# Kernel optimization log

Hardware: AMD Instinct MI355X
Metric: run time of the kernel (lower is better)

The kernel has to match this reference:

```python
import jax, jax.numpy as jnp
import numpy as np

B, S, D, H = 2, 2048, 1024, 16
HD = D // H  # 64
NEG = 1.0e9


def setup_inputs() -> dict:
    key = jax.random.key(0)
    ks = jax.random.split(key, 9)
    scale = 1.0 / np.sqrt(D)
    return {
        "q_in": jax.random.normal(ks[0], (B, S, D), jnp.float32),
        "k_in": jax.random.normal(ks[1], (B, S, D), jnp.float32),
        "v_in": jax.random.normal(ks[2], (B, S, D), jnp.float32),
        "Wq": jax.random.normal(ks[3], (D, D), jnp.float32) * scale,
        "bq": jnp.zeros((D,), jnp.float32),
        "Wk": jax.random.normal(ks[4], (D, D), jnp.float32) * scale,
        "bk": jnp.zeros((D,), jnp.float32),
        "Wv": jax.random.normal(ks[5], (D, D), jnp.float32) * scale,
        "bv": jnp.zeros((D,), jnp.float32),
        "Wo": jax.random.normal(ks[6], (D, D), jnp.float32) * scale,
        "bo": jnp.zeros((D,), jnp.float32),
    }


def _split_heads(x):
    # [B,S,D] -> [B,H,S,HD]
    return x.reshape(B, S, H, HD).transpose(0, 2, 1, 3)


def reference(q_in, k_in, v_in, Wq, bq, Wk, bk, Wv, bv, Wo, bo):
    q = _split_heads(q_in @ Wq + bq)
    k = _split_heads(k_in @ Wk + bk)
    v = _split_heads(v_in @ Wv + bv)
    # scaled dot-product attention with additive causal mask (use_causal_mask=True)
    scores = jnp.einsum("bhqd,bhkd->bhqk", q, k) / jnp.sqrt(jnp.float32(HD))
    causal = jnp.tril(jnp.ones((S, S), jnp.float32))  # band_part(ones, -1, 0)
    scores = scores + (causal - 1.0) * NEG
    weights = jax.nn.softmax(scores, axis=-1)
    attn = jnp.einsum("bhqk,bhkd->bhqd", weights, v)
    concat = attn.transpose(0, 2, 1, 3).reshape(B, S, D)
    return concat @ Wo + bo
```

## Files before the change

kernel.cpp:

```cpp
#include <hip/hip_runtime.h>

#define B_  2
#define S_  2048
#define D_  1024
#define H_  16
#define HD_ 64
#define MM  (B_ * S_)

typedef __bf16 bf16;
typedef __attribute__((ext_vector_type(8))) __bf16 bf16x8;
typedef __attribute__((ext_vector_type(4))) __bf16 bf16x4;
typedef __attribute__((ext_vector_type(4))) float  f32x4;

__device__ inline float exp2g(float x) { return __builtin_amdgcn_exp2f(x); }

__device__ inline bf16x8 load8(const bf16* p) { return *(const bf16x8*)p; }
__device__ inline bf16x8 load8(const float* p) {
  float4 a = *(const float4*)p;
  float4 b = *(const float4*)(p + 4);
  bf16x8 r;
  r[0] = (bf16)a.x; r[1] = (bf16)a.y; r[2] = (bf16)a.z; r[3] = (bf16)a.w;
  r[4] = (bf16)b.x; r[5] = (bf16)b.y; r[6] = (bf16)b.z; r[7] = (bf16)b.w;
  return r;
}

__device__ inline void gld16(void* lds, const void* g) {
  __builtin_amdgcn_global_load_lds(
      (const __attribute__((address_space(1))) unsigned int*)g,
      (__attribute__((address_space(3))) unsigned int*)lds, 16, 0, 0);
}

__global__ __launch_bounds__(256) void transpose_w(
    const float* __restrict__ W0, const float* __restrict__ W1,
    const float* __restrict__ W2, const float* __restrict__ W3,
    bf16* __restrict__ T0, bf16* __restrict__ T1,
    bf16* __restrict__ T2, bf16* __restrict__ T3,
    const float* __restrict__ X0, const float* __restrict__ X1,
    const float* __restrict__ X2,
    bf16* __restrict__ Y0, bf16* __restrict__ Y1, bf16* __restrict__ Y2) {
  const int z = blockIdx.z;
  if (z >= 4) {
    const int p = z - 4, t = p >> 2;
    const float* src = t == 0 ? X0 : t == 1 ? X1 : X2;
    bf16* dst = t == 0 ? Y0 : t == 1 ? Y1 : Y2;
    long base = ((long)(p & 3) << 20) +
                (long)(blockIdx.y * 32 + blockIdx.x) * 1024 + threadIdx.x * 4;
    float4 v = *(const float4*)&src[base];
    bf16x4 o4;
    o4[0] = (bf16)v.x; o4[1] = (bf16)v.y; o4[2] = (bf16)v.z; o4[3] = (bf16)v.w;
    *(bf16x4*)&dst[base] = o4;
    return;
  }
  __shared__ bf16 t[32][40];
  const float* in = z == 0 ? W0 : z == 1 ? W1 : z == 2 ? W2 : W3;
  bf16* out = z == 0 ? T0 : z == 1 ? T1 : z == 2 ? T2 : T3;
  const int tx = threadIdx.x & 31;
  const int ty = threadIdx.x >> 5;
  const int r0 = blockIdx.y * 32, c0 = blockIdx.x * 32;
#pragma unroll
  for (int j = 0; j < 32; j += 8)
    t[ty + j][tx] = (bf16)in[(long)(r0 + ty + j) * D_ + (c0 + tx)];
  __syncthreads();
#pragma unroll
  for (int j = 0; j < 32; j += 8)
    out[(long)(c0 + ty + j) * D_ + (r0 + tx)] = t[tx][ty + j];
}

__global__ __launch_bounds__(256) void transpose_v64(const bf16* __restrict__ V,
                                                     bf16* __restrict__ VT) {
  __shared__ bf16 t[64][72];
  const int tid = threadIdx.x;
  const int s0 = blockIdx.x * 64;
  const int bh = blockIdx.y;
  const int b = bh >> 4, h = bh & 15;
  const bf16* ip = V + (long)b * S_ * D_ + h * HD_;
  bf16* op = VT + (long)bh * HD_ * S_;
#pragma unroll
  for (int i = 0; i < 2; ++i) {
    int c = tid + i * 256;
    int r = c >> 3, cc = (c & 7) * 8;
    *(bf16x8*)&t[r][cc] = *(const bf16x8*)&ip[(long)(s0 + r) * D_ + cc];
  }
  __syncthreads();
#pragma unroll
  for (int i = 0; i < 2; ++i) {
    int c = tid + i * 256;
    int d = c >> 3, sc = (c & 7) * 8;
    bf16x8 v;
#pragma unroll
    for (int j = 0; j < 8; ++j) v[j] = t[sc + j][d];
    *(bf16x8*)&op[(long)d * S_ + s0 + sc] = v;
  }
}

template <typename AT, typename OT>
__global__ __launch_bounds__(256) void gemm_bt_dma(
    const AT* __restrict__ A0, const AT* __restrict__ A1, const AT* __restrict__ A2,
    const bf16* __restrict__ B0, const bf16* __restrict__ B1, const bf16* __restrict__ B2,
    const float* __restrict__ c0, const float* __restrict__ c1, const float* __restrict__ c2,
    OT* __restrict__ C0, OT* __restrict__ C1, OT* __restrict__ C2,
    int M, int N, int K) {
  __shared__ bf16 lA[128][32];
  __shared__ bf16 lB[128][32];
  const int z = blockIdx.z;
  const AT*    A    = z == 0 ? A0 : z == 1 ? A1 : A2;
  const bf16*  Bt   = z == 0 ? B0 : z == 1 ? B1 : B2;
  const float* bias = z == 0 ? c0 : z == 1 ? c1 : c2;
  OT*          C    = z == 0 ? C0 : z == 1 ? C1 : C2;

  const int tid = threadIdx.x;
  const int lane = tid & 63, wave = tid >> 6;
  const int quad = lane >> 4, l16 = lane & 15;
  const int bm = blockIdx.y * 128, bn = blockIdx.x * 128;
  const int wm = (wave >> 1) * 64, wn = (wave & 1) * 64;

  f32x4 acc[4][4] = {};

  for (int k0 = 0; k0 < K; k0 += 32) {
    __syncthreads();
#pragma unroll
    for (int i = 0; i < 2; ++i) {
      const int nbase = wave * 128 + i * 64;
      const int n = nbase + lane;
      const int row = n >> 2, kc = (n & 3) * 8;
      gld16(&lB[0][0] + (long)nbase * 8, &Bt[(long)(bn + row) * K + k0 + kc]);
      if constexpr (__is_same(AT, bf16))
        gld16(&lA[0][0] + (long)nbase * 8, &A[(long)(bm + row) * K + k0 + kc]);
    }
    if constexpr (!__is_same(AT, bf16)) {
#pragma unroll
      for (int i = 0; i < 2; ++i) {
        int c = tid + i * 256;
        int row = c >> 2, kc = (c & 3) * 8;
        *(bf16x8*)&lA[row][kc] = load8(&A[(long)(bm + row) * K + k0 + kc]);
      }
    }
    __syncthreads();
    bf16x8 af[4], bfr[4];
#pragma unroll
    for (int i = 0; i < 4; ++i) {
      af[i]  = *(const bf16x8*)&lA[wm + i * 16 + l16][quad * 8];
      bfr[i] = *(const bf16x8*)&lB[wn + i * 16 + l16][quad * 8];
    }
#pragma unroll
    for (int mi = 0; mi < 4; ++mi)
#pragma unroll
      for (int ni = 0; ni < 4; ++ni)
        acc[mi][ni] = __builtin_amdgcn_mfma_f32_16x16x32_bf16(af[mi], bfr[ni],
                                                              acc[mi][ni], 0, 0, 0);
  }

#pragma unroll
  for (int mi = 0; mi < 4; ++mi)
#pragma unroll
    for (int ni = 0; ni < 4; ++ni) {
      int col = bn + wn + ni * 16 + l16;
      float bv = bias[col];
#pragma unroll
      for (int r = 0; r < 4; ++r) {
        int row = bm + wm + mi * 16 + quad * 4 + r;
        C[(long)row * N + col] = (OT)(acc[mi][ni][r] + bv);
      }
    }
}

#define SCALE_LOG2E 0.1803368801111244f

__device__ inline void attn_step3(bool diag, int qloc, int quad, int l16,
                                  const bf16 (*lKb)[64], const bf16 (*lVb)[64],
                                  bf16 (*lpw)[72], const bf16x8* aq,
                                  f32x4* o, float& m_s, float& l_s) {
  const int sw = l16 & 7;
  f32x4 s[4];
#pragma unroll
  for (int ni = 0; ni < 4; ++ni) {
    f32x4 a = {};
#pragma unroll
    for (int c = 0; c < 2; ++c) {
      bf16x8 kf = *(const bf16x8*)&lKb[ni * 16 + l16][((c * 4 + quad) ^ sw) * 8];
      a = __builtin_amdgcn_mfma_f32_16x16x32_bf16(kf, aq[c], a, 0, 0, 0);
    }
    s[ni] = a * SCALE_LOG2E;
  }
  if (diag) {
#pragma unroll
    for (int ni = 0; ni < 4; ++ni)
#pragma unroll
      for (int r = 0; r < 4; ++r)
        if (ni * 16 + quad * 4 + r > qloc) s[ni][r] = -1e9f;
  }
  f32x4 m4 = s[0];
#pragma unroll
  for (int ni = 1; ni < 4; ++ni)
#pragma unroll
    for (int r = 0; r < 4; ++r) m4[r] = fmaxf(m4[r], s[ni][r]);
  float mx = fmaxf(fmaxf(m4[0], m4[1]), fmaxf(m4[2], m4[3]));
  mx = fmaxf(mx, __shfl_xor(mx, 16));
  mx = fmaxf(mx, __shfl_xor(mx, 32));
  float mn = fmaxf(m_s, mx);
  float alpha = exp2g(m_s - mn);
  m_s = mn;
  float rs = 0.f;
#pragma unroll
  for (int ni = 0; ni < 4; ++ni)
#pragma unroll
    for (int r = 0; r < 4; ++r) {
      float p = exp2g(s[ni][r] - mn);
      s[ni][r] = p;
      rs += p;
    }
  rs += __shfl_xor(rs, 16);
  rs += __shfl_xor(rs, 32);
  l_s = l_s * alpha + rs;
#pragma unroll
  for (int ni = 0; ni < 4; ++ni)
#pragma unroll
    for (int r = 0; r < 4; ++r)
      lpw[l16][ni * 16 + quad * 4 + r] = (bf16)s[ni][r];
#pragma unroll
  for (int di = 0; di < 4; ++di) o[di] *= alpha;
#pragma unroll
  for (int c = 0; c < 2; ++c) {
    bf16x8 ap = *(const bf16x8*)&lpw[l16][c * 32 + quad * 8];
#pragma unroll
    for (int di = 0; di < 4; ++di) {
      bf16x8 vf = *(const bf16x8*)&lVb[di * 16 + l16][((c * 4 + quad) ^ sw) * 8];
      o[di] = __builtin_amdgcn_mfma_f32_16x16x32_bf16(vf, ap, o[di], 0, 0, 0);
    }
  }
}

__device__ inline void store_o(bf16* Ob, int qrow, int lane, int quad, int l16,
                               bf16 (*lpw)[72], const f32x4* o, float l_s) {
  const float inv = 1.0f / l_s;
#pragma unroll
  for (int di = 0; di < 4; ++di)
#pragma unroll
    for (int r = 0; r < 4; ++r)
      lpw[l16][di * 16 + quad * 4 + r] = (bf16)(o[di][r] * inv);
  const int q = lane >> 2, db = (lane & 3) * 16;
  bf16x8 v0 = *(const bf16x8*)&lpw[q][db];
  bf16x8 v1 = *(const bf16x8*)&lpw[q][db + 8];
  *(bf16x8*)&Ob[(long)(qrow + q) * D_ + db] = v0;
  *(bf16x8*)&Ob[(long)(qrow + q) * D_ + db + 8] = v1;
}

__global__ __launch_bounds__(256) void flash_attn3(const bf16* __restrict__ Q,
                                                   const bf16* __restrict__ K,
                                                   const bf16* __restrict__ VT,
                                                   bf16* __restrict__ O) {
  __shared__ bf16 lK[2][64][64];
  __shared__ bf16 lV[2][64][64];
  __shared__ bf16 lp[4][16][72];
  const int tid = threadIdx.x;
  const int lane = tid & 63, wave = tid >> 6;
  const int quad = lane >> 4, l16 = lane & 15;
  const int x = blockIdx.x, bh = blockIdx.y;
  const int qtA = x, qtB = 31 - x;
  const int b = bh >> 4, h = bh & 15;
  const bf16* Qb = Q + (long)b * S_ * D_ + h * HD_;
  const bf16* Kb = K + (long)b * S_ * D_ + h * HD_;
  const bf16* Vb = VT + (long)bh * HD_ * S_;
  const int qrowA = qtA * 64 + wave * 16;
  const int qrowB = qtB * 64 + wave * 16;
  const int qloc = wave * 16 + l16;

  bf16x8 aqA[2], aqB[2];
#pragma unroll
  for (int c = 0; c < 2; ++c) {
    aqA[c] = *(const bf16x8*)&Qb[(long)(qrowA + l16) * D_ + c * 32 + quad * 8];
    aqB[c] = *(const bf16x8*)&Qb[(long)(qrowB + l16) * D_ + c * 32 + quad * 8];
  }

  f32x4 oA[4] = {}, oB[4] = {};
  float mA = -1e30f, lA_ = 0.f, mB = -1e30f, lB_ = 0.f;

  const int srow = tid >> 3, scol = tid & 7;
  const int swcol0 = (scol ^ (srow & 7)) * 8;
  const int srow1 = srow + 32;
  const int swcol1 = (scol ^ (srow1 & 7)) * 8;

  bf16x8 kreg[2], vreg[2];
  kreg[0] = *(const bf16x8*)&Kb[(long)srow * D_ + scol * 8];
  kreg[1] = *(const bf16x8*)&Kb[(long)srow1 * D_ + scol * 8];
  vreg[0] = *(const bf16x8*)&Vb[(long)srow * S_ + scol * 8];
  vreg[1] = *(const bf16x8*)&Vb[(long)srow1 * S_ + scol * 8];
  *(bf16x8*)&lK[0][srow][swcol0]  = kreg[0];
  *(bf16x8*)&lK[0][srow1][swcol1] = kreg[1];
  *(bf16x8*)&lV[0][srow][swcol0]  = vreg[0];
  *(bf16x8*)&lV[0][srow1][swcol1] = vreg[1];
  __syncthreads();

  const int ktMax = qtB;
  for (int kt = 0; kt <= ktMax; ++kt) {
    const int p = kt & 1;
    if (kt < ktMax) {
      const long k0 = (long)(kt + 1) * 64;
      kreg[0] = *(const bf16x8*)&Kb[(k0 + srow) * D_ + scol * 8];
      kreg[1] = *(const bf16x8*)&Kb[(k0 + srow1) * D_ + scol * 8];
      vreg[0] = *(const bf16x8*)&Vb[(long)srow * S_ + k0 + scol * 8];
      vreg[1] = *(const bf16x8*)&Vb[(long)srow1 * S_ + k0 + scol * 8];
    }
    attn_step3(kt == qtB, qloc, quad, l16, lK[p], lV[p], lp[wave], aqB, oB, mB, lB_);
    if (kt <= qtA)
      attn_step3(kt == qtA, qloc, quad, l16, lK[p], lV[p], lp[wave], aqA, oA, mA, lA_);
    if (kt < ktMax) {
      *(bf16x8*)&lK[1 - p][srow][swcol0]  = kreg[0];
      *(bf16x8*)&lK[1 - p][srow1][swcol1] = kreg[1];
      *(bf16x8*)&lV[1 - p][srow][swcol0]  = vreg[0];
      *(bf16x8*)&lV[1 - p][srow1][swcol1] = vreg[1];
      __syncthreads();
    }
  }

  bf16* Ob = O + (long)b * S_ * D_ + h * HD_;
  store_o(Ob, qrowA, lane, quad, l16, lp[wave], oA, lA_);
  store_o(Ob, qrowB, lane, quad, l16, lp[wave], oB, lB_);
}

extern "C" void kernel_launch(void* const* d_in, const int* in_sizes, int n_in,
                              void* d_out, int out_size, void* d_ws, size_t ws_size,
                              hipStream_t stream) {
  (void)in_sizes; (void)n_in; (void)out_size;
  const float* q_in = (const float*)d_in[0];
  const float* k_in = (const float*)d_in[1];
  const float* v_in = (const float*)d_in[2];
  const float* Wq   = (const float*)d_in[3];
  const float* bq   = (const float*)d_in[4];
  const float* Wk   = (const float*)d_in[5];
  const float* bk   = (const float*)d_in[6];
  const float* Wv   = (const float*)d_in[7];
  const float* bv   = (const float*)d_in[8];
  const float* Wo   = (const float*)d_in[9];
  const float* bo   = (const float*)d_in[10];
  float* out = (float*)d_out;

  bf16* ws = (bf16*)d_ws;
  const size_t WSZ = (size_t)D_ * D_;
  const size_t TSZ = (size_t)B_ * S_ * D_;
  bf16* WqT = ws;
  bf16* WkT = WqT + WSZ;
  bf16* WvT = WkT + WSZ;
  bf16* WoT = WvT + WSZ;
  bf16* Qp  = WoT + WSZ;
  bf16* Kp  = Qp + TSZ;
  bf16* Vp  = Kp + TSZ;
  bf16* VTp = Vp + TSZ;
  bf16* Ap  = VTp + TSZ;
  bf16* Xq  = VTp;
  bf16* Xk  = Ap;
  bf16* Xv  = Ap + TSZ;
  const bool pre = ws_size >= (4 * WSZ + 6 * TSZ) * sizeof(bf16);

  dim3 blk(256);
  transpose_w<<<dim3(32, 32, pre ? 16 : 4), blk, 0, stream>>>(
      Wq, Wk, Wv, Wo, WqT, WkT, WvT, WoT, q_in, k_in, v_in, Xq, Xk, Xv);

  if (pre)
    gemm_bt_dma<bf16, bf16><<<dim3(8, 32, 3), blk, 0, stream>>>(
        Xq, Xk, Xv, WqT, WkT, WvT, bq, bk, bv, Qp, Kp, Vp, MM, D_, D_);
  else
    gemm_bt_dma<float, bf16><<<dim3(8, 32, 3), blk, 0, stream>>>(
        q_in, k_in, v_in, WqT, WkT, WvT, bq, bk, bv, Qp, Kp, Vp, MM, D_, D_);

  transpose_v64<<<dim3(S_ / 64, B_ * H_), blk, 0, stream>>>(Vp, VTp);

  flash_attn3<<<dim3(16, B_ * H_), blk, 0, stream>>>(Qp, Kp, VTp, Ap);

  gemm_bt_dma<bf16, float><<<dim3(8, 32, 1), blk, 0, stream>>>(
      Ap, Ap, Ap, WoT, WoT, WoT, bo, bo, bo, out, out, out, MM, D_, D_);
}
```

Measured before the change: 240.6 us.

## Split attention q-tile pairs across 8 waves and use smaller-tile output GEMM

The flash attention kernel now launches 512 threads per block. Waves 0-3 handle the low query tile and waves 4-7 the high query tile, instead of each wave running both tiles in sequence. This halves per-wave serial work and register pressure, and doubles the threads sharing each K/V tile load. The output projection uses a new GEMM with a 128x64 tile, doubling the block count to improve occupancy on the small M×N. P and O writes to LDS are also vectorized to bf16x4. The cost is that waves 0-3 sit idle at the barriers while the longer B tile is still running.

Result: faster. 231.2 us (-3.9%).

```diff
diff --git a/kernel.cpp b/kernel.cpp
--- a/kernel.cpp
+++ b/kernel.cpp
@@ -164,9 +164,69 @@
     }
 }
 
+__global__ __launch_bounds__(256) void gemm_bt_64(const bf16* __restrict__ A,
+                                                  const bf16* __restrict__ Bt,
+                                                  const float* __restrict__ bias,
+                                                  float* __restrict__ C,
+                                                  int M, int N, int K) {
+  __shared__ bf16 lA[128][32];
+  __shared__ bf16 lB[64][32];
+  const int tid = threadIdx.x;
+  const int lane = tid & 63, wave = tid >> 6;
+  const int quad = lane >> 4, l16 = lane & 15;
+  const int bm = blockIdx.y * 128, bn = blockIdx.x * 64;
+  const int wm = (wave >> 1) * 64, wn = (wave & 1) * 32;
+
+  f32x4 acc[4][2] = {};
+
+  for (int k0 = 0; k0 < K; k0 += 32) {
+    __syncthreads();
+#pragma unroll
+    for (int i = 0; i < 2; ++i) {
+      const int nbase = wave * 128 + i * 64;
+      const int n = nbase + lane;
+      const int row = n >> 2, kc = (n & 3) * 8;
+      gld16(&lA[0][0] + (long)nbase * 8, &A[(long)(bm + row) * K + k0 + kc]);
+    }
+    {
+      const int nbase = wave * 64;
+      const int n = nbase + lane;
+      const int row = n >> 2, kc = (n & 3) * 8;
+      gld16(&lB[0][0] + (long)nbase * 8, &Bt[(long)(bn + row) * K + k0 + kc]);
+    }
+    __syncthreads();
+    bf16x8 af[4], bfr[2];
+#pragma unroll
+    for (int i = 0; i < 4; ++i)
+      af[i] = *(const bf16x8*)&lA[wm + i * 16 + l16][quad * 8];
+#pragma unroll
+    for (int i = 0; i < 2; ++i)
+      bfr[i] = *(const bf16x8*)&lB[wn + i * 16 + l16][quad * 8];
+#pragma unroll
+    for (int mi = 0; mi < 4; ++mi)
+#pragma unroll
+      for (int ni = 0; ni < 2; ++ni)
+        acc[mi][ni] = __builtin_amdgcn_mfma_f32_16x16x32_bf16(af[mi], bfr[ni],
+                                                              acc[mi][ni], 0, 0, 0);
+  }
+
+#pragma unroll
+  for (int mi = 0; mi < 4; ++mi)
+#pragma unroll
+    for (int ni = 0; ni < 2; ++ni) {
+      int col = bn + wn + ni * 16 + l16;
+      float bv = bias[col];
+#pragma unroll
+      for (int r = 0; r < 4; ++r) {
+        int row = bm + wm + mi * 16 + quad * 4 + r;
+        C[(long)row * N + col] = acc[mi][ni][r] + bv;
+      }
+    }
+}
+
 #define SCALE_LOG2E 0.1803368801111244f
 
-__device__ inline void attn_step3(bool diag, int qloc, int quad, int l16,
+__device__ inline void attn_step4(bool diag, int qloc, int quad, int l16,
                                   const bf16 (*lKb)[64], const bf16 (*lVb)[64],
                                   bf16 (*lpw)[72], const bf16x8* aq,
                                   f32x4* o, float& m_s, float& l_s) {
@@ -213,10 +273,12 @@
   rs += __shfl_xor(rs, 32);
   l_s = l_s * alpha + rs;
 #pragma unroll
-  for (int ni = 0; ni < 4; ++ni)
-#pragma unroll
-    for (int r = 0; r < 4; ++r)
-      lpw[l16][ni * 16 + quad * 4 + r] = (bf16)s[ni][r];
+  for (int ni = 0; ni < 4; ++ni) {
+    bf16x4 p4;
+#pragma unroll
+    for (int r = 0; r < 4; ++r) p4[r] = (bf16)s[ni][r];
+    *(bf16x4*)&lpw[l16][ni * 16 + quad * 4] = p4;
+  }
 #pragma unroll
   for (int di = 0; di < 4; ++di) o[di] *= alpha;
 #pragma unroll
@@ -234,10 +296,12 @@
                                bf16 (*lpw)[72], const f32x4* o, float l_s) {
   const float inv = 1.0f / l_s;
 #pragma unroll
-  for (int di = 0; di < 4; ++di)
-#pragma unroll
-    for (int r = 0; r < 4; ++r)
-      lpw[l16][di * 16 + quad * 4 + r] = (bf16)(o[di][r] * inv);
+  for (int di = 0; di < 4; ++di) {
+    bf16x4 p4;
+#pragma unroll
+    for (int r = 0; r < 4; ++r) p4[r] = (bf16)(o[di][r] * inv);
+    *(bf16x4*)&lpw[l16][di * 16 + quad * 4] = p4;
+  }
   const int q = lane >> 2, db = (lane & 3) * 16;
   bf16x8 v0 = *(const bf16x8*)&lpw[q][db];
   bf16x8 v1 = *(const bf16x8*)&lpw[q][db + 8];
@@ -245,50 +309,44 @@
   *(bf16x8*)&Ob[(long)(qrow + q) * D_ + db + 8] = v1;
 }
 
-__global__ __launch_bounds__(256) void flash_attn3(const bf16* __restrict__ Q,
+__global__ __launch_bounds__(512) void flash_attn4(const bf16* __restrict__ Q,
                                                    const bf16* __restrict__ K,
                                                    const bf16* __restrict__ VT,
                                                    bf16* __restrict__ O) {
   __shared__ bf16 lK[2][64][64];
   __shared__ bf16 lV[2][64][64];
-  __shared__ bf16 lp[4][16][72];
+  __shared__ bf16 lp[8][16][72];
   const int tid = threadIdx.x;
   const int lane = tid & 63, wave = tid >> 6;
   const int quad = lane >> 4, l16 = lane & 15;
   const int x = blockIdx.x, bh = blockIdx.y;
   const int qtA = x, qtB = 31 - x;
+  const bool isB = wave >= 4;
+  const int w4 = wave & 3;
+  const int myqt = isB ? qtB : qtA;
   const int b = bh >> 4, h = bh & 15;
   const bf16* Qb = Q + (long)b * S_ * D_ + h * HD_;
   const bf16* Kb = K + (long)b * S_ * D_ + h * HD_;
   const bf16* Vb = VT + (long)bh * HD_ * S_;
-  const int qrowA = qtA * 64 + wave * 16;
-  const int qrowB = qtB * 64 + wave * 16;
-  const int qloc = wave * 16 + l16;
-
-  bf16x8 aqA[2], aqB[2];
-#pragma unroll
-  for (int c = 0; c < 2; ++c) {
-    aqA[c] = *(const bf16x8*)&Qb[(long)(qrowA + l16) * D_ + c * 32 + quad * 8];
-    aqB[c] = *(const bf16x8*)&Qb[(long)(qrowB + l16) * D_ + c * 32 + quad * 8];
-  }
-
-  f32x4 oA[4] = {}, oB[4] = {};
-  float mA = -1e30f, lA_ = 0.f, mB = -1e30f, lB_ = 0.f;
+  const int qrow = myqt * 64 + w4 * 16;
+  const int qloc = w4 * 16 + l16;
+
+  bf16x8 aq[2];
+#pragma unroll
+  for (int c = 0; c < 2; ++c)
+    aq[c] = *(const bf16x8*)&Qb[(long)(qrow + l16) * D_ + c * 32 + quad * 8];
+
+  f32x4 o[4] = {};
+  float m_s = -1e30f, l_s = 0.f;
 
   const int srow = tid >> 3, scol = tid & 7;
-  const int swcol0 = (scol ^ (srow & 7)) * 8;
-  const int srow1 = srow + 32;
-  const int swcol1 = (scol ^ (srow1 & 7)) * 8;
-
-  bf16x8 kreg[2], vreg[2];
-  kreg[0] = *(const bf16x8*)&Kb[(long)srow * D_ + scol * 8];
-  kreg[1] = *(const bf16x8*)&Kb[(long)srow1 * D_ + scol * 8];
-  vreg[0] = *(const bf16x8*)&Vb[(long)srow * S_ + scol * 8];
-  vreg[1] = *(const bf16x8*)&Vb[(long)srow1 * S_ + scol * 8];
-  *(bf16x8*)&lK[0][srow][swcol0]  = kreg[0];
-  *(bf16x8*)&lK[0][srow1][swcol1] = kreg[1];
-  *(bf16x8*)&lV[0][srow][swcol0]  = vreg[0];
-  *(bf16x8*)&lV[0][srow1][swcol1] = vreg[1];
+  const int swcol = (scol ^ (srow & 7)) * 8;
+
+  bf16x8 kreg, vreg;
+  kreg = *(const bf16x8*)&Kb[(long)srow * D_ + scol * 8];
+  vreg = *(const bf16x8*)&Vb[(long)srow * S_ + scol * 8];
+  *(bf16x8*)&lK[0][srow][swcol] = kreg;
+  *(bf16x8*)&lV[0][srow][swcol] = vreg;
   __syncthreads();
 
   const int ktMax = qtB;
@@ -296,26 +354,21 @@
     const int p = kt & 1;
     if (kt < ktMax) {
       const long k0 = (long)(kt + 1) * 64;
-      kreg[0] = *(const bf16x8*)&Kb[(k0 + srow) * D_ + scol * 8];
-      kreg[1] = *(const bf16x8*)&Kb[(k0 + srow1) * D_ + scol * 8];
-      vreg[0] = *(const bf16x8*)&Vb[(long)srow * S_ + k0 + scol * 8];
-      vreg[1] = *(const bf16x8*)&Vb[(long)srow1 * S_ + k0 + scol * 8];
-    }
-    attn_step3(kt == qtB, qloc, quad, l16, lK[p], lV[p], lp[wave], aqB, oB, mB, lB_);
-    if (kt <= qtA)
-      attn_step3(kt == qtA, qloc, quad, l16, lK[p], lV[p], lp[wave], aqA, oA, mA, lA_);
+      kreg = *(const bf16x8*)&Kb[(k0 + srow) * D_ + scol * 8];
+      vreg = *(const bf16x8*)&Vb[(long)srow * S_ + k0 + scol * 8];
+    }
+    if (isB || kt <= qtA)
+      attn_step4(kt == myqt, qloc, quad, l16, lK[p], lV[p], lp[wave], aq,
+                 o, m_s, l_s);
     if (kt < ktMax) {
-      *(bf16x8*)&lK[1 - p][srow][swcol0]  = kreg[0];
-      *(bf16x8*)&lK[1 - p][srow1][swcol1] = kreg[1];
-      *(bf16x8*)&lV[1 - p][srow][swcol0]  = vreg[0];
-      *(bf16x8*)&lV[1 - p][srow1][swcol1] = vreg[1];
+      *(bf16x8*)&lK[1 - p][srow][swcol] = kreg;
+      *(bf16x8*)&lV[1 - p][srow][swcol] = vreg;
       __syncthreads();
     }
   }
 
   bf16* Ob = O + (long)b * S_ * D_ + h * HD_;
-  store_o(Ob, qrowA, lane, quad, l16, lp[wave], oA, lA_);
-  store_o(Ob, qrowB, lane, quad, l16, lp[wave], oB, lB_);
+  store_o(Ob, qrow, lane, quad, l16, lp[wave], o, l_s);
 }
 
 extern "C" void kernel_launch(void* const* d_in, const int* in_sizes, int n_in,
@@ -365,8 +418,7 @@
 
   transpose_v64<<<dim3(S_ / 64, B_ * H_), blk, 0, stream>>>(Vp, VTp);
 
-  flash_attn3<<<dim3(16, B_ * H_), blk, 0, stream>>>(Qp, Kp, VTp, Ap);
-
-  gemm_bt_dma<bf16, float><<<dim3(8, 32, 1), blk, 0, stream>>>(
-      Ap, Ap, Ap, WoT, WoT, WoT, bo, bo, bo, out, out, out, MM, D_, D_);
-}
+  flash_attn4<<<dim3(16, B_ * H_), dim3(512), 0, stream>>>(Qp, Kp, VTp, Ap);
+
+  gemm_bt_64<<<dim3(16, 32), blk, 0, stream>>>(Ap, WoT, bo, out, MM, D_, D_);
+}
```
